# Performance work log

Hardware: AMD Instinct MI355X
Metric: run time of the kernel (lower is better)

## Reference

```python
import jax, jax.numpy as jnp
import numpy as np

B, C, L, H, K, NCONV = 16, 128, 1024, 8, 7, 4
DK = C // H
EPS = 1e-5
NEG = -1e30


def setup_inputs() -> dict:
    key = jax.random.key(0)
    ks = jax.random.split(key, 20)
    s = 0.05
    rn = lambda k, shape: jax.random.normal(k, shape, jnp.float32) * s
    return {
        "x": jax.random.normal(ks[0], (B, C, L), jnp.float32),
        "mask": jax.random.bernoulli(ks[1], 0.1, (B, L)),
        "dw_w": rn(ks[2], (NCONV, C, K)),
        "pw_w": rn(ks[3], (NCONV, C, C)),
        "pw_b": rn(ks[4], (NCONV, C)),
        "ng": jnp.ones((NCONV + 2, C), jnp.float32),
        "nb": jnp.zeros((NCONV + 2, C), jnp.float32),
        "wq": rn(ks[5], (C, C)), "bq": rn(ks[6], (C,)),
        "wk": rn(ks[7], (C, C)), "bk": rn(ks[8], (C,)),
        "wv": rn(ks[9], (C, C)), "bv": rn(ks[10], (C,)),
        "wo": rn(ks[11], (C, C)), "bo": rn(ks[12], (C,)),
        "w1": rn(ks[13], (C, C)), "b1": rn(ks[14], (C,)),
        "w2": rn(ks[15], (C, C)), "b2": rn(ks[16], (C,)),
    }


def _pos_encoding(c, length):
    i = jnp.arange(c, dtype=jnp.float32)
    even = (jnp.arange(c) % 2) == 0
    freq = jnp.where(even, jnp.power(10000.0, -i / c), -jnp.power(10000.0, (1.0 - i) / c))
    phase = jnp.where(even, 0.0, jnp.pi / 2)
    pos = jnp.arange(length, dtype=jnp.float32)
    return jnp.sin(pos[None, :] * freq[:, None] + phase[:, None])  # [C, L]


def _ln(x, g, b):
    # layer norm over channel dim of [B, C, L]
    mu = jnp.mean(x, axis=1, keepdims=True)
    var = jnp.mean(jnp.square(x - mu), axis=1, keepdims=True)
    xn = (x - mu) * jax.lax.rsqrt(var + EPS)
    return xn * g[None, :, None] + b[None, :, None]


def _dsconv(x, dw, pw, pb):
    # depthwise conv1d (groups=C, pad k//2, no bias) + pointwise conv1d (bias)
    y = jax.lax.conv_general_dilated(
        x, dw[:, None, :], window_strides=(1,), padding=[(K // 2, K // 2)],
        feature_group_count=C, dimension_numbers=("NCH", "OIH", "NCH"))
    return jnp.einsum("oc,bcl->bol", pw, y) + pb[None, :, None]


def _attention(x, mask, wq, bq, wk, bk, wv, bv, wo, bo):
    # x: [B, C, L] -> [B, L, C]
    xt = jnp.swapaxes(x, 1, 2)
    q = (xt @ wq.T + bq).reshape(B, L, H, DK)
    k = (xt @ wk.T + bk).reshape(B, L, H, DK)
    v = (xt @ wv.T + bv).reshape(B, L, H, DK)
    scale = 1.0 / np.sqrt(DK)
    scores = jnp.einsum("blhd,bmhd->bhlm", q, k) * scale  # [B, H, L, L]
    scores = jnp.where(mask[:, None, None, :], NEG, scores)
    attn = jax.nn.softmax(scores, axis=-1)
    out = jnp.einsum("bhlm,bmhd->blhd", attn, v).reshape(B, L, C)
    out = out @ wo.T + bo
    return jnp.swapaxes(out, 1, 2)  # [B, C, L]


def reference(x, mask, dw_w, pw_w, pw_b, ng, nb, wq, bq, wk, bk, wv, bv, wo, bo, w1, b1, w2, b2):
    # eval mode: all dropout / stochastic depth are identity
    out = x + _pos_encoding(C, L)[None]
    for i in range(NCONV):
        res = out
        out = _ln(out, ng[i], nb[i])
        out = _dsconv(out, dw_w[i], pw_w[i], pw_b[i])
        out = jax.nn.relu(out)
        out = out + res
    res = out
    out = _ln(out, ng[NCONV], nb[NCONV])
    out = _attention(out, mask, wq, bq, wk, bk, wv, bv, wo, bo)
    out = out + res
    res = out
    out = _ln(out, ng[NCONV + 1], nb[NCONV + 1])
    ot = jnp.swapaxes(out, 1, 2)
    ot = jax.nn.relu(ot @ w1.T + b1)
    ot = ot @ w2.T + b2
    out = jnp.swapaxes(ot, 1, 2) + res
    return out
```

## Files before the change

kernel.cpp:

```cpp
#include <hip/hip_runtime.h>
#include <math.h>


#define ACT_N   2097152
#define OFF_ACT0 0
#define OFF_ACT1 (ACT_N)
#define OFF_QB   (2*ACT_N)
#define OFF_KB   (3*ACT_N)
#define OFF_VT   (4*ACT_N)
#define OFF_ABF  (5*ACT_N)
#define OFF_MF   (6*ACT_N)
#define OFF_WB   (6*ACT_N + 16384)
#define OFF_DW8  (6*ACT_N + 16384 + 81920)

typedef __attribute__((ext_vector_type(8)))  short bf16x8;
typedef __attribute__((ext_vector_type(16))) float f32x16;
typedef __attribute__((ext_vector_type(4)))  float f32x4;

static __device__ __forceinline__ unsigned int f2bf(float f) {
    unsigned int u = __float_as_uint(f);
    return (u + 0x7fffu + ((u >> 16) & 1u)) >> 16;
}
static __device__ __forceinline__ unsigned int pk2(float a, float b) {
    return f2bf(a) | (f2bf(b) << 16);
}

#define GOFF(row, g) (((row) << 8) + ((((g) ^ ((row) & 15))) << 4))

#define QSCALE 0.3606737602222409f

__global__ __launch_bounds__(256) void k_prep(
    const float* __restrict__ pw, const float* __restrict__ wq,
    const float* __restrict__ wk, const float* __restrict__ wv_,
    const float* __restrict__ wo, const float* __restrict__ w1,
    const float* __restrict__ w2, const unsigned char* __restrict__ mask,
    const float* __restrict__ dwsrc,
    unsigned short* __restrict__ wb, float* __restrict__ maskf,
    float* __restrict__ dw8)
{
    int blk = blockIdx.x, t = threadIdx.x;
    if (blk < 10) {
        const float* src;
        if (blk < 4)       src = pw + blk * 16384;
        else if (blk == 4) src = wq;
        else if (blk == 5) src = wk;
        else if (blk == 6) src = wv_;
        else if (blk == 7) src = wo;
        else if (blk == 8) src = w1;
        else               src = w2;
        unsigned short* dst = wb + blk * 16384;
        for (int i = t * 8; i < 16384; i += 2048) {
            float4 a = *(const float4*)(src + i);
            float4 c = *(const float4*)(src + i + 4);
            uint4 v;
            v.x = pk2(a.x, a.y); v.y = pk2(a.z, a.w);
            v.z = pk2(c.x, c.y); v.w = pk2(c.z, c.w);
            *(uint4*)(dst + i) = v;
        }
    } else if (blk == 10) {
        for (int i = t; i < 16384; i += 256)
            maskf[i] = mask[i] ? -3.0e38f : 0.0f;
    } else {
        for (int i = t; i < 4096; i += 256) {
            int n = i >> 3, tap = i & 7;
            dw8[i] = (tap < 7) ? dwsrc[n * 7 + tap] : 0.0f;
        }
    }
}

__global__ __launch_bounds__(256) void k_pe(const float* __restrict__ x,
                                            float* __restrict__ out)
{
    int i4 = blockIdx.x * 256 + threadIdx.x;
    int base = i4 * 4;
    int l = base & 1023;
    int c = (base >> 10) & 127;
    float e = (float)(c & ~1);
    float fb = exp2f(e * (-13.287712379549449f / 128.0f));
    float freq = (c & 1) ? -fb : fb;
    float ph   = (c & 1) ? 1.5707963267948966f : 0.0f;
    float4 xv = ((const float4*)x)[i4];
    float4 o;
    o.x = xv.x + sinf((float)l * freq + ph);
    o.y = xv.y + sinf((float)(l + 1) * freq + ph);
    o.z = xv.z + sinf((float)(l + 2) * freq + ph);
    o.w = xv.w + sinf((float)(l + 3) * freq + ph);
    ((float4*)out)[i4] = o;
}

__global__ __launch_bounds__(512) void k_conv(
    const float* __restrict__ in, float* __restrict__ out,
    const unsigned short* __restrict__ wb,
    const float* __restrict__ dw8,
    const float* __restrict__ pb,
    const float* __restrict__ g, const float* __restrict__ nbv)
{
    __shared__ unsigned short Wl[16384];
    __shared__ unsigned short Xl[8192];
    __shared__ float part[560];
    __shared__ float muL[70], rsL[70];

    const int b  = blockIdx.x >> 4;
    const int l0 = (blockIdx.x & 15) << 6;
    const int t  = threadIdx.x;
    const int lane = t & 63;
    const int w = __builtin_amdgcn_readfirstlane(t >> 6);
    const float* xb = in + b * 131072;

    {
        const uint4* src = (const uint4*)wb;
        #pragma unroll
        for (int i = 0; i < 4; ++i) {
            int gi = t + i * 512;
            uint4 v = src[gi];
            int row = gi >> 4, c16 = gi & 15;
            *(uint4*)((char*)Wl + GOFF(row, c16)) = v;
        }
    }
    if (t < 280) {
        int col = t >> 2, sl = t & 3;
        int gl = l0 - 3 + col;
        float s = 0.f, ss = 0.f;
        if ((unsigned)gl < 1024u) {
            for (int c = sl * 32; c < sl * 32 + 32; ++c) {
                float v = xb[c * 1024 + gl];
                s += v; ss = fmaf(v, v, ss);
            }
        }
        part[col * 8 + sl * 2]     = s;
        part[col * 8 + sl * 2 + 1] = ss;
    }
    __syncthreads();
    if (t < 70) {
        int gl = l0 - 3 + t;
        if ((unsigned)gl < 1024u) {
            float s  = part[t*8] + part[t*8+2] + part[t*8+4] + part[t*8+6];
            float ss = part[t*8+1] + part[t*8+3] + part[t*8+5] + part[t*8+7];
            float mu = s * 0.0078125f;
            float var = ss * 0.0078125f - mu * mu;
            muL[t] = mu; rsL[t] = rsqrtf(var + 1e-5f);
        } else { muL[t] = 0.f; rsL[t] = 0.f; }
    }
    __syncthreads();

    {
        const int l = lane;
        const int gl = l0 + l;
        float m[7], rf[7], vm[7];
        int pofs[7];
        #pragma unroll
        for (int j = 0; j < 7; ++j) {
            int p = gl - 3 + j;
            m[j]  = muL[l + j];
            rf[j] = rsL[l + j];
            vm[j] = ((unsigned)p < 1024u) ? 1.f : 0.f;
            pofs[j] = min(max(p, 0), 1023);
        }
        #pragma unroll
        for (int s = 0; s < 2; ++s) {
            int c0 = w * 16 + s * 8;
            unsigned int pk[4];
            #pragma unroll
            for (int cp = 0; cp < 4; ++cp) {
                float y2[2];
                #pragma unroll
                for (int ci = 0; ci < 2; ++ci) {
                    int c = c0 + cp * 2 + ci;
                    const float* xr = xb + c * 1024;
                    const float* dr = dw8 + c * 8;
                    float S1 = 0.f, S2 = 0.f;
                    #pragma unroll
                    for (int j = 0; j < 7; ++j) {
                        float xv = xr[pofs[j]];
                        float u = (xv - m[j]) * rf[j];
                        float dwv = dr[j];
                        S1 = fmaf(dwv, u,     S1);
                        S2 = fmaf(dwv, vm[j], S2);
                    }
                    y2[ci] = g[c] * S1 + nbv[c] * S2;
                }
                pk[cp] = pk2(y2[0], y2[1]);
            }
            *(uint4*)((char*)Xl + GOFF(l, (c0 >> 3))) = *(uint4*)pk;
        }
    }
    __syncthreads();

    const int l31 = lane & 31, hi = lane >> 5;
    const int ow = w >> 1, lh = w & 1;
    bf16x8 af[8];
    #pragma unroll
    for (int kc = 0; kc < 8; ++kc)
        af[kc] = *(const bf16x8*)((char*)Wl + GOFF(ow * 32 + l31, kc * 2 + hi));
    f32x16 acc;
    #pragma unroll
    for (int i = 0; i < 16; ++i) acc[i] = 0.f;
    #pragma unroll
    for (int kc = 0; kc < 8; ++kc) {
        bf16x8 bx = *(const bf16x8*)((char*)Xl + GOFF(lh * 32 + l31, kc * 2 + hi));
        acc = __builtin_amdgcn_mfma_f32_32x32x16_bf16(af[kc], bx, acc, 0, 0, 0);
    }
    float* ob = out + b * 131072;
    const int lg = l0 + lh * 32 + l31;
    #pragma unroll
    for (int r = 0; r < 16; ++r) {
        int o = ow * 32 + (r & 3) + 8 * (r >> 2) + 4 * hi;
        ob[o * 1024 + lg] = fmaxf(acc[r] + pb[o], 0.f) + xb[o * 1024 + lg];
    }
}

__global__ __launch_bounds__(512) void k_qkv(
    const float* __restrict__ in, const unsigned short* __restrict__ wb,
    const float* __restrict__ bq, const float* __restrict__ bk,
    const float* __restrict__ bv,
    const float* __restrict__ g, const float* __restrict__ nbv,
    unsigned short* __restrict__ qb, unsigned short* __restrict__ kb,
    unsigned short* __restrict__ vt)
{
    __shared__ unsigned short Wl[16384];
    __shared__ unsigned short Xl[8192];
    __shared__ unsigned short vs[8][1280];
    __shared__ float part[1024];
    __shared__ float muL[64], rsL[64];

    const int b  = blockIdx.x >> 4;
    const int l0 = (blockIdx.x & 15) << 6;
    const int t  = threadIdx.x;
    const int lane = t & 63;
    const int w = __builtin_amdgcn_readfirstlane(t >> 6);
    const float* xb = in + b * 131072;

    {
        const uint4* src = (const uint4*)wb;
        #pragma unroll
        for (int i = 0; i < 4; ++i) {
            int gi = t + i * 512;
            uint4 v = src[gi];
            int row = gi >> 4, c16 = gi & 15;
            *(uint4*)((char*)Wl + GOFF(row, c16)) = v;
        }
    }
    {
        int col = t >> 3, sl = t & 7;
        float s = 0.f, ss = 0.f;
        for (int c = sl * 16; c < sl * 16 + 16; ++c) {
            float v = xb[c * 1024 + l0 + col];
            s += v; ss = fmaf(v, v, ss);
        }
        part[col * 16 + sl * 2]     = s;
        part[col * 16 + sl * 2 + 1] = ss;
    }
    __syncthreads();
    if (t < 64) {
        float s = 0.f, ss = 0.f;
        #pragma unroll
        for (int j = 0; j < 8; ++j) { s += part[t*16 + j*2]; ss += part[t*16 + j*2 + 1]; }
        float mu = s * 0.0078125f;
        float var = ss * 0.0078125f - mu * mu;
        muL[t] = mu; rsL[t] = rsqrtf(var + 1e-5f);
    }
    __syncthreads();
    {
        const int l = lane;
        float mu = muL[l], rs = rsL[l];
        #pragma unroll
        for (int s = 0; s < 2; ++s) {
            int c0 = w * 16 + s * 8;
            unsigned int pk[4];
            #pragma unroll
            for (int cp = 0; cp < 4; ++cp) {
                int c = c0 + cp * 2;
                float v0 = (xb[c * 1024 + l0 + l]       - mu) * rs * g[c]     + nbv[c];
                float v1 = (xb[(c + 1) * 1024 + l0 + l] - mu) * rs * g[c + 1] + nbv[c + 1];
                pk[cp] = pk2(v0, v1);
            }
            *(uint4*)((char*)Xl + GOFF(l, (c0 >> 3))) = *(uint4*)pk;
        }
    }
    __syncthreads();

    const int l31 = lane & 31, hi = lane >> 5;
    const int ow = w >> 1, lh = w & 1;
    const int lg = l0 + lh * 32 + l31;

    for (int p = 0; p < 3; ++p) {
        uint4 pw4[4];
        if (p < 2) {
            const uint4* src = (const uint4*)(wb + (p + 1) * 16384);
            #pragma unroll
            for (int i = 0; i < 4; ++i) pw4[i] = src[t + i * 512];
        }
        bf16x8 af[8];
        #pragma unroll
        for (int kc = 0; kc < 8; ++kc)
            af[kc] = *(const bf16x8*)((char*)Wl + GOFF(ow * 32 + l31, kc * 2 + hi));
        f32x16 acc;
        #pragma unroll
        for (int i = 0; i < 16; ++i) acc[i] = 0.f;
        #pragma unroll
        for (int kc = 0; kc < 8; ++kc) {
            bf16x8 bx = *(const bf16x8*)((char*)Xl + GOFF(lh * 32 + l31, kc * 2 + hi));
            acc = __builtin_amdgcn_mfma_f32_32x32x16_bf16(af[kc], bx, acc, 0, 0, 0);
        }

        if (p < 2) {
            const float* bias = (p == 0) ? bq : bk;
            unsigned short* dst = (p == 0) ? qb : kb;
            const float scl = (p == 0) ? QSCALE : 1.0f;
            unsigned int pk0[4], pk1[4];
            #pragma unroll
            for (int j2 = 0; j2 < 4; ++j2) {
                int r = j2 * 2;
                int o0 = ow * 32 + (r & 3) + 8 * (r >> 2) + 4 * hi;
                pk0[j2] = pk2((acc[r] + bias[o0]) * scl,
                              (acc[r + 1] + bias[o0 + 1]) * scl);
                int r8 = r + 8;
                int o1 = ow * 32 + (r8 & 3) + 8 * (r8 >> 2) + 4 * hi;
                pk1[j2] = pk2((acc[r8] + bias[o1]) * scl,
                              (acc[r8 + 1] + bias[o1 + 1]) * scl);
            }
            int bh0 = b * 8 + 2 * ow;
            *(uint4*)(dst + ((size_t)bh0 * 1024 + lg) * 16 + hi * 8) = *(uint4*)pk0;
            *(uint4*)(dst + ((size_t)(bh0 + 1) * 1024 + lg) * 16 + hi * 8) = *(uint4*)pk1;
        } else {
            unsigned short* vsw = vs[w];
            #pragma unroll
            for (int r = 0; r < 16; ++r) {
                int orow = (r & 3) + 8 * (r >> 2) + 4 * hi;
                int o = ow * 32 + orow;
                vsw[orow * 40 + l31] = (unsigned short)f2bf(acc[r] + bv[o]);
            }
            int d32 = l31;
            uint4 v0 = *(uint4*)(vsw + d32 * 40 + hi * 16);
            uint4 v1 = *(uint4*)(vsw + d32 * 40 + hi * 16 + 8);
            int head = 2 * ow + (d32 >> 4), dd = d32 & 15;
            unsigned short* vp = vt + ((size_t)(b * 8 + head) * 16 + dd) * 1024
                                    + l0 + lh * 32 + hi * 16;
            *(uint4*)vp = v0; *(uint4*)(vp + 8) = v1;
        }
        __syncthreads();
        if (p < 2) {
            #pragma unroll
            for (int i = 0; i < 4; ++i) {
                int gi = t + i * 512;
                int row = gi >> 4, c16 = gi & 15;
                *(uint4*)((char*)Wl + GOFF(row, c16)) = pw4[i];
            }
            __syncthreads();
        }
    }
}

__global__ __launch_bounds__(256) void k_attn(
    const unsigned short* __restrict__ qb, const unsigned short* __restrict__ kb,
    const unsigned short* __restrict__ vt, const float* __restrict__ madd,
    unsigned short* __restrict__ abf)
{
    __shared__ unsigned short Kl[4096];
    __shared__ unsigned short Vl[4224];
    __shared__ float Ml[1024];
    __shared__ unsigned int Pl[4][640];

    const int bh = blockIdx.x >> 3;
    const int b  = bh >> 3;
    const int h  = bh & 7;
    const int qbase = (blockIdx.x & 7) << 7;
    const int t = threadIdx.x;
    const int lane = t & 63;
    const int w = t >> 6;
    const int l31 = lane & 31, hi = lane >> 5;
    const int l15 = lane & 15, h2 = lane >> 4;
    const int qw = qbase + w * 32;

    const uint4* ksrc = (const uint4*)(kb + (size_t)bh * 16384);
    const unsigned short* vsrc = vt + (size_t)bh * 16384;

    const int d0v = t >> 5,          ko0 = t & 31;
    const int d1v = (t + 256) >> 5,  ko1 = (t + 256) & 31;
    const int kp0 = t & 1,        kk0 = t >> 1;
    const int kp1 = t & 1,        kk1 = (t + 256) >> 1;

    ((float4*)Ml)[t] = ((const float4*)(madd + b * 1024))[t];

    bf16x8 qf;
    {
        uint4 qv = *(const uint4*)(qb + ((size_t)bh * 1024 + qw + l31) * 16 + hi * 8);
        union { uint4 u; bf16x8 v; } cvt; cvt.u = qv; qf = cvt.v;
    }
    bf16x8 ones;
    #pragma unroll
    for (int i = 0; i < 8; ++i) ones[i] = (short)0x3F80;

    {
        uint4 kr0 = ksrc[t], kr1 = ksrc[t + 256];
        uint4 vr0 = *(const uint4*)(vsrc + d0v * 1024 + ko0 * 8);
        uint4 vr1 = *(const uint4*)(vsrc + d1v * 1024 + ko1 * 8);
        *(uint4*)(&Kl[kp0 * 2048 + kk0 * 8]) = kr0;
        *(uint4*)(&Kl[kp1 * 2048 + kk1 * 8]) = kr1;
        *(uint4*)(&Vl[d0v * 264 + ko0 * 8]) = vr0;
        *(uint4*)(&Vl[d1v * 264 + ko1 * 8]) = vr1;
    }
    __syncthreads();

    f32x16 Z;
    #pragma unroll
    for (int i = 0; i < 16; ++i) Z[i] = 0.f;
    f32x4 O0, O1, Os0, Os1;
    #pragma unroll
    for (int i = 0; i < 4; ++i) { O0[i] = 0.f; O1[i] = 0.f; Os0[i] = 0.f; Os1[i] = 0.f; }

    unsigned int* myP = &Pl[w][0];

    for (int ch = 0; ch < 4; ++ch) {
        uint4 kr0, kr1, vr0, vr1;
        if (ch < 3) {
            int cb = (ch + 1) * 512;
            int vb = (ch + 1) * 256;
            kr0 = ksrc[cb + t];
            kr1 = ksrc[cb + t + 256];
            vr0 = *(const uint4*)(vsrc + d0v * 1024 + vb + ko0 * 8);
            vr1 = *(const uint4*)(vsrc + d1v * 1024 + vb + ko1 * 8);
        }
        const int kgbase = ch * 256;

        #pragma unroll
        for (int kc = 0; kc < 8; ++kc) {
            bf16x8 kf = *(const bf16x8*)(Kl + hi * 2048 + (kc * 32 + l31) * 8);
            f32x16 S = __builtin_amdgcn_mfma_f32_32x32x16_bf16(kf, qf, Z, 0, 0, 0);

            #pragma unroll
            for (int rg = 0; rg < 4; ++rg) {
                float4 mm = *(const float4*)(Ml + kgbase + kc * 32 + rg * 8 + hi * 4);
                float p0 = __builtin_amdgcn_exp2f(S[rg * 4 + 0] + mm.x);
                float p1 = __builtin_amdgcn_exp2f(S[rg * 4 + 1] + mm.y);
                float p2 = __builtin_amdgcn_exp2f(S[rg * 4 + 2] + mm.z);
                float p3 = __builtin_amdgcn_exp2f(S[rg * 4 + 3] + mm.w);
                uint2 pwd;
                pwd.x = __builtin_amdgcn_perm(__float_as_uint(p1),
                                              __float_as_uint(p0), 0x07060302u);
                pwd.y = __builtin_amdgcn_perm(__float_as_uint(p3),
                                              __float_as_uint(p2), 0x07060302u);
                *(uint2*)((char*)myP + l31 * 80 + rg * 16 + hi * 8) = pwd;
            }

            bf16x8 vf  = *(const bf16x8*)(Vl + l15 * 264 + kc * 32 + h2 * 8);
            bf16x8 pa0 = *(const bf16x8*)((const char*)myP + l15 * 80 + h2 * 16);
            bf16x8 pa1 = *(const bf16x8*)((const char*)myP + (16 + l15) * 80 + h2 * 16);
            __builtin_amdgcn_s_setprio(1);
            O0  = __builtin_amdgcn_mfma_f32_16x16x32_bf16(pa0, vf,   O0,  0, 0, 0);
            O1  = __builtin_amdgcn_mfma_f32_16x16x32_bf16(pa1, vf,   O1,  0, 0, 0);
            Os0 = __builtin_amdgcn_mfma_f32_16x16x32_bf16(pa0, ones, Os0, 0, 0, 0);
            Os1 = __builtin_amdgcn_mfma_f32_16x16x32_bf16(pa1, ones, Os1, 0, 0, 0);
            __builtin_amdgcn_s_setprio(0);
        }

        if (ch < 3) {
            __syncthreads();
            *(uint4*)(&Kl[kp0 * 2048 + kk0 * 8]) = kr0;
            *(uint4*)(&Kl[kp1 * 2048 + kk1 * 8]) = kr1;
            *(uint4*)(&Vl[d0v * 264 + ko0 * 8]) = vr0;
            *(uint4*)(&Vl[d1v * 264 + ko1 * 8]) = vr1;
            __syncthreads();
        }
    }

    unsigned short* myP16 = (unsigned short*)myP;
    #pragma unroll
    for (int r = 0; r < 4; ++r) {
        float i0 = __builtin_amdgcn_rcpf(Os0[r] + 1e-37f);
        float i1 = __builtin_amdgcn_rcpf(Os1[r] + 1e-37f);
        myP16[(h2 * 4 + r) * 20 + l15]        = (unsigned short)f2bf(O0[r] * i0);
        myP16[(16 + h2 * 4 + r) * 20 + l15]   = (unsigned short)f2bf(O1[r] * i1);
    }
    uint4 ov = *(const uint4*)(myP16 + l31 * 20 + hi * 8);
    *(uint4*)(abf + ((size_t)(b * 1024 + qw + l31)) * 128 + h * 16 + hi * 8) = ov;
}

__global__ __launch_bounds__(512) void k_oproj(
    const unsigned short* __restrict__ abf, const unsigned short* __restrict__ wb,
    const float* __restrict__ bo, const float* __restrict__ res,
    float* __restrict__ out)
{
    __shared__ unsigned short Wl[16384];
    __shared__ unsigned short Xl[8192];
    const int b  = blockIdx.x >> 4;
    const int l0 = (blockIdx.x & 15) << 6;
    const int t  = threadIdx.x;
    const int lane = t & 63;
    const int w = __builtin_amdgcn_readfirstlane(t >> 6);

    {
        const uint4* src = (const uint4*)wb;
        #pragma unroll
        for (int i = 0; i < 4; ++i) {
            int gi = t + i * 512;
            uint4 v = src[gi];
            int row = gi >> 4, c16 = gi & 15;
            *(uint4*)((char*)Wl + GOFF(row, c16)) = v;
        }
        #pragma unroll
        for (int i = 0; i < 2; ++i) {
            int gi = t + i * 512;
            int row = gi >> 4, c16 = gi & 15;
            uint4 v = *(const uint4*)(abf + ((size_t)(b * 1024 + l0 + row)) * 128 + c16 * 8);
            *(uint4*)((char*)Xl + GOFF(row, c16)) = v;
        }
    }
    __syncthreads();

    const int l31 = lane & 31, hi = lane >> 5;
    const int ow = w >> 1, lh = w & 1;
    bf16x8 af[8];
    #pragma unroll
    for (int kc = 0; kc < 8; ++kc)
        af[kc] = *(const bf16x8*)((char*)Wl + GOFF(ow * 32 + l31, kc * 2 + hi));
    f32x16 acc;
    #pragma unroll
    for (int i = 0; i < 16; ++i) acc[i] = 0.f;
    #pragma unroll
    for (int kc = 0; kc < 8; ++kc) {
        bf16x8 bx = *(const bf16x8*)((char*)Xl + GOFF(lh * 32 + l31, kc * 2 + hi));
        acc = __builtin_amdgcn_mfma_f32_32x32x16_bf16(af[kc], bx, acc, 0, 0, 0);
    }
    const float* rb = res + b * 131072;
    float* ob = out + b * 131072;
    const int lg = l0 + lh * 32 + l31;
    #pragma unroll
    for (int r = 0; r < 16; ++r) {
        int o = ow * 32 + (r & 3) + 8 * (r >> 2) + 4 * hi;
        ob[o * 1024 + lg] = acc[r] + bo[o] + rb[o * 1024 + lg];
    }
}

__global__ __launch_bounds__(512) void k_ffn(
    const float* __restrict__ in,
    const unsigned short* __restrict__ w1b, const unsigned short* __restrict__ w2b,
    const float* __restrict__ b1, const float* __restrict__ b2,
    const float* __restrict__ g, const float* __restrict__ nbv,
    float* __restrict__ out)
{
    __shared__ unsigned short Wl[16384];
    __shared__ unsigned short Xl[8192];
    __shared__ unsigned short Xl2[8192];
    __shared__ float part[1024];
    __shared__ float muL[64], rsL[64];

    const int b  = blockIdx.x >> 4;
    const int l0 = (blockIdx.x & 15) << 6;
    const int t  = threadIdx.x;
    const int lane = t & 63;
    const int w = __builtin_amdgcn_readfirstlane(t >> 6);
    const float* xb = in + b * 131072;

    {
        const uint4* src = (const uint4*)w1b;
        #pragma unroll
        for (int i = 0; i < 4; ++i) {
            int gi = t + i * 512;
            uint4 v = src[gi];
            int row = gi >> 4, c16 = gi & 15;
            *(uint4*)((char*)Wl + GOFF(row, c16)) = v;
        }
    }
    {
        int col = t >> 3, sl = t & 7;
        float s = 0.f, ss = 0.f;
        for (int c = sl * 16; c < sl * 16 + 16; ++c) {
            float v = xb[c * 1024 + l0 + col];
            s += v; ss = fmaf(v, v, ss);
        }
        part[col * 16 + sl * 2]     = s;
        part[col * 16 + sl * 2 + 1] = ss;
    }
    __syncthreads();
    if (t < 64) {
        float s = 0.f, ss = 0.f;
        #pragma unroll
        for (int j = 0; j < 8; ++j) { s += part[t*16 + j*2]; ss += part[t*16 + j*2 + 1]; }
        float mu = s * 0.0078125f;
        float var = ss * 0.0078125f - mu * mu;
        muL[t] = mu; rsL[t] = rsqrtf(var + 1e-5f);
    }
    __syncthreads();
    {
        const int l = lane;
        float mu = muL[l], rs = rsL[l];
        #pragma unroll
        for (int s = 0; s < 2; ++s) {
            int c0 = w * 16 + s * 8;
            unsigned int pk[4];
            #pragma unroll
            for (int cp = 0; cp < 4; ++cp) {
                int c = c0 + cp * 2;
                float v0 = (xb[c * 1024 + l0 + l]       - mu) * rs * g[c]     + nbv[c];
                float v1 = (xb[(c + 1) * 1024 + l0 + l] - mu) * rs * g[c + 1] + nbv[c + 1];
                pk[cp] = pk2(v0, v1);
            }
            *(uint4*)((char*)Xl + GOFF(l, (c0 >> 3))) = *(uint4*)pk;
        }
    }
    __syncthreads();

    const int l31 = lane & 31, hi = lane >> 5;
    const int ow = w >> 1, lh = w & 1;
    const int lrow = lh * 32 + l31;

    uint4 pw4[4];
    {
        const uint4* src = (const uint4*)w2b;
        #pragma unroll
        for (int i = 0; i < 4; ++i) pw4[i] = src[t + i * 512];
    }
    {
        bf16x8 af[8];
        #pragma unroll
        for (int kc = 0; kc < 8; ++kc)
            af[kc] = *(const bf16x8*)((char*)Wl + GOFF(ow * 32 + l31, kc * 2 + hi));
        f32x16 acc;
        #pragma unroll
        for (int i = 0; i < 16; ++i) acc[i] = 0.f;
        #pragma unroll
        for (int kc = 0; kc < 8; ++kc) {
            bf16x8 bx = *(const bf16x8*)((char*)Xl + GOFF(lrow, kc * 2 + hi));
            acc = __builtin_amdgcn_mfma_f32_32x32x16_bf16(af[kc], bx, acc, 0, 0, 0);
        }
        #pragma unroll
        for (int r = 0; r < 16; ++r) {
            int o = ow * 32 + (r & 3) + 8 * (r >> 2) + 4 * hi;
            float hval = fmaxf(acc[r] + b1[o], 0.f);
            *(unsigned short*)((char*)Xl2 + (lrow << 8)
                + ((((o >> 3) ^ (lrow & 15))) << 4) + ((o & 7) * 2)) =
                (unsigned short)f2bf(hval);
        }
    }
    __syncthreads();
    {
        #pragma unroll
        for (int i = 0; i < 4; ++i) {
            int gi = t + i * 512;
            int row = gi >> 4, c16 = gi & 15;
            *(uint4*)((char*)Wl + GOFF(row, c16)) = pw4[i];
        }
    }
    __syncthreads();
    {
        bf16x8 af[8];
        #pragma unroll
        for (int kc = 0; kc < 8; ++kc)
            af[kc] = *(const bf16x8*)((char*)Wl + GOFF(ow * 32 + l31, kc * 2 + hi));
        f32x16 acc;
        #pragma unroll
        for (int i = 0; i < 16; ++i) acc[i] = 0.f;
        #pragma unroll
        for (int kc = 0; kc < 8; ++kc) {
            bf16x8 bx = *(const bf16x8*)((char*)Xl2 + GOFF(lrow, kc * 2 + hi));
            acc = __builtin_amdgcn_mfma_f32_32x32x16_bf16(af[kc], bx, acc, 0, 0, 0);
        }
        float* ob = out + b * 131072;
        const int lg = l0 + lrow;
        #pragma unroll
        for (int r = 0; r < 16; ++r) {
            int o = ow * 32 + (r & 3) + 8 * (r >> 2) + 4 * hi;
            ob[o * 1024 + lg] = acc[r] + b2[o] + xb[o * 1024 + lg];
        }
    }
}

extern "C" void kernel_launch(void* const* d_in, const int* in_sizes, int n_in,
                              void* d_out, int out_size, void* d_ws, size_t ws_size,
                              hipStream_t stream)
{
    const float* x    = (const float*)d_in[0];
    const unsigned char* mask = (const unsigned char*)d_in[1];
    const float* dw_w = (const float*)d_in[2];
    const float* pw_w = (const float*)d_in[3];
    const float* pw_b = (const float*)d_in[4];
    const float* ng   = (const float*)d_in[5];
    const float* nb   = (const float*)d_in[6];
    const float* wq   = (const float*)d_in[7];
    const float* bq   = (const float*)d_in[8];
    const float* wk   = (const float*)d_in[9];
    const float* bk   = (const float*)d_in[10];
    const float* wv   = (const float*)d_in[11];
    const float* bv   = (const float*)d_in[12];
    const float* wo   = (const float*)d_in[13];
    const float* bo   = (const float*)d_in[14];
    const float* w1   = (const float*)d_in[15];
    const float* b1   = (const float*)d_in[16];
    const float* w2   = (const float*)d_in[17];
    const float* b2   = (const float*)d_in[18];

    float* ws   = (float*)d_ws;
    float* act0 = ws + OFF_ACT0;
    float* act1 = ws + OFF_ACT1;
    unsigned short* qb  = (unsigned short*)(ws + OFF_QB);
    unsigned short* kbp = (unsigned short*)(ws + OFF_KB);
    unsigned short* vtp = (unsigned short*)(ws + OFF_VT);
    unsigned short* abf = (unsigned short*)(ws + OFF_ABF);
    float* mf   = ws + OFF_MF;
    unsigned short* wb = (unsigned short*)(ws + OFF_WB);
    float* dw8  = ws + OFF_DW8;

    k_prep<<<12, 256, 0, stream>>>(pw_w, wq, wk, wv, wo, w1, w2, mask, dw_w,
                                   wb, mf, dw8);
    k_pe<<<2048, 256, 0, stream>>>(x, act0);

    k_conv<<<256, 512, 0, stream>>>(act0, act1, wb + 0 * 16384, dw8 + 0,
                                    pw_b + 0,   ng + 0,   nb + 0);
    k_conv<<<256, 512, 0, stream>>>(act1, act0, wb + 1 * 16384, dw8 + 1024,
                                    pw_b + 128, ng + 128, nb + 128);
    k_conv<<<256, 512, 0, stream>>>(act0, act1, wb + 2 * 16384, dw8 + 2048,
                                    pw_b + 256, ng + 256, nb + 256);
    k_conv<<<256, 512, 0, stream>>>(act1, act0, wb + 3 * 16384, dw8 + 3072,
                                    pw_b + 384, ng + 384, nb + 384);

    k_qkv<<<256, 512, 0, stream>>>(act0, wb + 4 * 16384, bq, bk, bv,
                                   ng + 4 * 128, nb + 4 * 128, qb, kbp, vtp);
    k_attn<<<1024, 256, 0, stream>>>(qb, kbp, vtp, mf, abf);
    k_oproj<<<256, 512, 0, stream>>>(abf, wb + 7 * 16384, bo, act0, act1);
    k_ffn<<<256, 512, 0, stream>>>(act1, wb + 8 * 16384, wb + 9 * 16384,
                                   b1, b2, ng + 5 * 128, nb + 5 * 128,
                                   (float*)d_out);
}
```

Baseline: 211.5 us.

## Keep softmax probabilities in registers and use 32x32 MFMA for PV

```diff
diff --git a/kernel.cpp b/kernel.cpp
--- a/kernel.cpp
+++ b/kernel.cpp
@@ -359,7 +359,7 @@
     __shared__ unsigned short Kl[4096];
     __shared__ unsigned short Vl[4224];
     __shared__ float Ml[1024];
-    __shared__ unsigned int Pl[4][640];
+    __shared__ float Sc[4][640];
 
     const int bh = blockIdx.x >> 3;
     const int b  = bh >> 3;
@@ -369,8 +369,8 @@
     const int lane = t & 63;
     const int w = t >> 6;
     const int l31 = lane & 31, hi = lane >> 5;
-    const int l15 = lane & 15, h2 = lane >> 4;
     const int qw = qbase + w * 32;
+    const bool hiB = (hi != 0);
 
     const uint4* ksrc = (const uint4*)(kb + (size_t)bh * 16384);
     const unsigned short* vsrc = vt + (size_t)bh * 16384;
@@ -387,9 +387,6 @@
         uint4 qv = *(const uint4*)(qb + ((size_t)bh * 1024 + qw + l31) * 16 + hi * 8);
         union { uint4 u; bf16x8 v; } cvt; cvt.u = qv; qf = cvt.v;
     }
-    bf16x8 ones;
-    #pragma unroll
-    for (int i = 0; i < 8; ++i) ones[i] = (short)0x3F80;
 
     {
         uint4 kr0 = ksrc[t], kr1 = ksrc[t + 256];
@@ -405,11 +402,12 @@
     f32x16 Z;
     #pragma unroll
     for (int i = 0; i < 16; ++i) Z[i] = 0.f;
-    f32x4 O0, O1, Os0, Os1;
-    #pragma unroll
-    for (int i = 0; i < 4; ++i) { O0[i] = 0.f; O1[i] = 0.f; Os0[i] = 0.f; Os1[i] = 0.f; }
-
-    unsigned int* myP = &Pl[w][0];
+    f32x16 O;
+    #pragma unroll
+    for (int i = 0; i < 16; ++i) O[i] = 0.f;
+    float sum_acc = 0.f;
+
+    const unsigned short* Vrow = Vl + (l31 & 15) * 264;
 
     for (int ch = 0; ch < 4; ++ch) {
         uint4 kr0, kr1, vr0, vr1;
@@ -428,29 +426,51 @@
             bf16x8 kf = *(const bf16x8*)(Kl + hi * 2048 + (kc * 32 + l31) * 8);
             f32x16 S = __builtin_amdgcn_mfma_f32_32x32x16_bf16(kf, qf, Z, 0, 0, 0);
 
+            float p[16];
             #pragma unroll
             for (int rg = 0; rg < 4; ++rg) {
                 float4 mm = *(const float4*)(Ml + kgbase + kc * 32 + rg * 8 + hi * 4);
-                float p0 = __builtin_amdgcn_exp2f(S[rg * 4 + 0] + mm.x);
-                float p1 = __builtin_amdgcn_exp2f(S[rg * 4 + 1] + mm.y);
-                float p2 = __builtin_amdgcn_exp2f(S[rg * 4 + 2] + mm.z);
-                float p3 = __builtin_amdgcn_exp2f(S[rg * 4 + 3] + mm.w);
-                uint2 pwd;
-                pwd.x = __builtin_amdgcn_perm(__float_as_uint(p1),
-                                              __float_as_uint(p0), 0x07060302u);
-                pwd.y = __builtin_amdgcn_perm(__float_as_uint(p3),
-                                              __float_as_uint(p2), 0x07060302u);
-                *(uint2*)((char*)myP + l31 * 80 + rg * 16 + hi * 8) = pwd;
-            }
-
-            bf16x8 vf  = *(const bf16x8*)(Vl + l15 * 264 + kc * 32 + h2 * 8);
-            bf16x8 pa0 = *(const bf16x8*)((const char*)myP + l15 * 80 + h2 * 16);
-            bf16x8 pa1 = *(const bf16x8*)((const char*)myP + (16 + l15) * 80 + h2 * 16);
+                p[rg * 4 + 0] = __builtin_amdgcn_exp2f(S[rg * 4 + 0] + mm.x);
+                p[rg * 4 + 1] = __builtin_amdgcn_exp2f(S[rg * 4 + 1] + mm.y);
+                p[rg * 4 + 2] = __builtin_amdgcn_exp2f(S[rg * 4 + 2] + mm.z);
+                p[rg * 4 + 3] = __builtin_amdgcn_exp2f(S[rg * 4 + 3] + mm.w);
+            }
+
+            unsigned int u[8], s[8];
+            #pragma unroll
+            for (int m = 0; m < 8; ++m)
+                u[m] = __builtin_amdgcn_perm(__float_as_uint(p[2 * m + 1]),
+                                             __float_as_uint(p[2 * m]), 0x07060302u);
+            #pragma unroll
+            for (int m = 0; m < 8; ++m)
+                s[m] = __shfl_xor(u[m], 32);
+
+            {
+                float t0 = (p[0] + p[1]) + (p[2] + p[3]);
+                float t1 = (p[4] + p[5]) + (p[6] + p[7]);
+                float t2 = (p[8] + p[9]) + (p[10] + p[11]);
+                float t3 = (p[12] + p[13]) + (p[14] + p[15]);
+                sum_acc += (t0 + t1) + (t2 + t3);
+            }
+
+            unsigned int a0[4], a1[4];
+            a0[0] = hiB ? s[2] : u[0];
+            a0[1] = hiB ? s[3] : u[1];
+            a0[2] = hiB ? u[2] : s[0];
+            a0[3] = hiB ? u[3] : s[1];
+            a1[0] = hiB ? s[6] : u[4];
+            a1[1] = hiB ? s[7] : u[5];
+            a1[2] = hiB ? u[6] : s[4];
+            a1[3] = hiB ? u[7] : s[5];
+            union { unsigned int u4[4]; bf16x8 v; } c0, c1;
+            #pragma unroll
+            for (int i = 0; i < 4; ++i) { c0.u4[i] = a0[i]; c1.u4[i] = a1[i]; }
+
+            bf16x8 vf0 = *(const bf16x8*)(Vrow + kc * 32 + hi * 8);
+            bf16x8 vf1 = *(const bf16x8*)(Vrow + kc * 32 + 16 + hi * 8);
             __builtin_amdgcn_s_setprio(1);
-            O0  = __builtin_amdgcn_mfma_f32_16x16x32_bf16(pa0, vf,   O0,  0, 0, 0);
-            O1  = __builtin_amdgcn_mfma_f32_16x16x32_bf16(pa1, vf,   O1,  0, 0, 0);
-            Os0 = __builtin_amdgcn_mfma_f32_16x16x32_bf16(pa0, ones, Os0, 0, 0, 0);
-            Os1 = __builtin_amdgcn_mfma_f32_16x16x32_bf16(pa1, ones, Os1, 0, 0, 0);
+            O = __builtin_amdgcn_mfma_f32_32x32x16_bf16(c0.v, vf0, O, 0, 0, 0);
+            O = __builtin_amdgcn_mfma_f32_32x32x16_bf16(c1.v, vf1, O, 0, 0, 0);
             __builtin_amdgcn_s_setprio(0);
         }
 
@@ -464,16 +484,26 @@
         }
     }
 
-    unsigned short* myP16 = (unsigned short*)myP;
-    #pragma unroll
-    for (int r = 0; r < 4; ++r) {
-        float i0 = __builtin_amdgcn_rcpf(Os0[r] + 1e-37f);
-        float i1 = __builtin_amdgcn_rcpf(Os1[r] + 1e-37f);
-        myP16[(h2 * 4 + r) * 20 + l15]        = (unsigned short)f2bf(O0[r] * i0);
-        myP16[(16 + h2 * 4 + r) * 20 + l15]   = (unsigned short)f2bf(O1[r] * i1);
-    }
-    uint4 ov = *(const uint4*)(myP16 + l31 * 20 + hi * 8);
-    *(uint4*)(abf + ((size_t)(b * 1024 + qw + l31)) * 128 + h * 16 + hi * 8) = ov;
+    float total = sum_acc + __shfl_xor(sum_acc, 32);
+    float inv = __builtin_amdgcn_rcpf(total + 1e-37f);
+
+    float* sc = Sc[w];
+    if (l31 < 16) {
+        #pragma unroll
+        for (int r = 0; r < 16; ++r) {
+            int q = (r & 3) + 8 * (r >> 2) + 4 * hi;
+            sc[q * 20 + l31] = O[r];
+        }
+    }
+    float4 r0 = *(const float4*)(sc + l31 * 20 + hi * 8);
+    float4 r1 = *(const float4*)(sc + l31 * 20 + hi * 8 + 4);
+    unsigned int pk4[4];
+    pk4[0] = pk2(r0.x * inv, r0.y * inv);
+    pk4[1] = pk2(r0.z * inv, r0.w * inv);
+    pk4[2] = pk2(r1.x * inv, r1.y * inv);
+    pk4[3] = pk2(r1.z * inv, r1.w * inv);
+    *(uint4*)(abf + ((size_t)(b * 1024 + qw + l31)) * 128 + h * 16 + hi * 8) =
+        *(uint4*)pk4;
 }
 
 __global__ __launch_bounds__(512) void k_oproj(
```

After: 218.5 us. 1.03x slower.
